# Kernel optimization log

Hardware: AMD Instinct MI355X
Metric: run time of the kernel (lower is better)

Reference implementation:

```python
import jax, jax.numpy as jnp
import numpy as np
from jax import lax

NUM_HEADS = 4
KEY_DEPTHS = 32
ATTN_CH = 32
OUT_CH = 64
IN_CH = 32
KSIZE = 3


def circ_conv3d(x, w, b=None):
    # x: (B,C,D,H,W), w: (O,I,k,k,k); circular padding keeps spatial dims.
    k = w.shape[-1]
    p = k // 2
    if p > 0:
        x = jnp.pad(x, ((0, 0), (0, 0), (p, p), (p, p), (p, p)), mode='wrap')
    y = lax.conv_general_dilated(x, w, (1, 1, 1), 'VALID',
                                 dimension_numbers=('NCDHW', 'OIDHW', 'NCDHW'))
    if b is not None:
        y = y + b[None, :, None, None, None]
    return y


def setup_inputs() -> dict:
    key = jax.random.key(0)
    k1, k2, k3, k4, k5 = jax.random.split(key, 5)
    x = jax.random.normal(k1, (2, IN_CH, 16, 16, 16), dtype=jnp.float32)
    fan = IN_CH * KSIZE ** 3
    w_init = jax.random.normal(k2, (OUT_CH - ATTN_CH, IN_CH, KSIZE, KSIZE, KSIZE), dtype=jnp.float32) / np.sqrt(fan)
    w_qkv = jax.random.normal(k3, (2 * KEY_DEPTHS + ATTN_CH, IN_CH, KSIZE, KSIZE, KSIZE), dtype=jnp.float32) / np.sqrt(fan)
    w_out = jax.random.normal(k4, (ATTN_CH, ATTN_CH, 1, 1, 1), dtype=jnp.float32) / np.sqrt(ATTN_CH)
    b_out = jax.random.normal(k5, (ATTN_CH,), dtype=jnp.float32) * 0.01
    return {'x': x, 'w_init': w_init, 'w_qkv': w_qkv, 'w_out': w_out, 'b_out': b_out}


def reference(x, w_init, w_qkv, w_out, b_out):
    out = circ_conv3d(x, w_init)                      # (b, out-attn, w,h,d)
    b, _, w, h, d = out.shape
    qkv = circ_conv3d(x, w_qkv)                       # (b, 2dk+dv, w,h,d)
    q, k, v = jnp.split(qkv, [KEY_DEPTHS, 2 * KEY_DEPTHS], axis=1)
    dk_h = KEY_DEPTHS // NUM_HEADS
    dv_h = ATTN_CH // NUM_HEADS
    N = w * h * d
    scale = dk_h ** -0.5
    fq = q.reshape(b, NUM_HEADS, dk_h, N) * scale     # (b,H,dk_h,N)
    fk = k.reshape(b, NUM_HEADS, dk_h, N)
    fv = v.reshape(b, NUM_HEADS, dv_h, N)
    logits = jnp.einsum('bhcn,bhcm->bhnm', fq, fk)    # (b,H,N,N)
    weights = jax.nn.softmax(logits, axis=-1)
    attn = jnp.einsum('bhnm,bhvm->bhnv', weights, fv)  # (b,H,N,dv_h)
    # Faithful to torch: a pure reshape (memory reinterpretation), not a transpose.
    attn = attn.reshape(b, NUM_HEADS, dv_h, w, h, d)
    attn = attn.reshape(b, NUM_HEADS * dv_h, w, h, d)  # combine heads
    attn = circ_conv3d(attn, w_out, b_out)             # 1x1x1 conv
    return jnp.concatenate([out, attn], axis=1)
```

## Files before the change

### kernel.cpp

```cpp
#include <hip/hip_runtime.h>


typedef short short8 __attribute__((ext_vector_type(8)));
typedef float float4v __attribute__((ext_vector_type(4)));
typedef unsigned short ushort_t;
typedef unsigned int uint_t;

__device__ inline ushort_t f2bf(float x) {
  uint_t u = __builtin_bit_cast(uint_t, x);
  u += 0x7FFFu + ((u >> 16) & 1u);
  return (ushort_t)(u >> 16);
}

__device__ inline uint_t cvtpk(float lo, float hi) {
  uint_t r;
  asm("v_cvt_pk_bf16_f32 %0, %1, %2" : "=v"(r) : "v"(lo), "v"(hi));
  return r;
}

__global__ __launch_bounds__(256) void kPrep(const float* __restrict__ w_init,
                                             const float* __restrict__ w_qkv,
                                             const float* __restrict__ x,
                                             ushort_t* __restrict__ wA,
                                             ushort_t* __restrict__ xb) {
  __shared__ float xsf[256 * 34];
  int t = threadIdx.x;
  int bx = blockIdx.x;
  if (bx < 432) {
    int idx = bx * 256 + t;
    int j = idx & 7;
    int lane = (idx >> 3) & 63;
    int tap = (idx >> 9) % 27;
    int otile = idx / (27 * 512);
    int o = otile * 16 + (lane & 15);
    int ic = (lane >> 4) * 8 + j;
    const float QS = 0.35355339059327373f * 1.4426950408889634f;
    float v;
    if (o < 32) v = w_init[(o * 32 + ic) * 27 + tap];
    else        v = w_qkv[((o - 32) * 32 + ic) * 27 + tap];
    if (o >= 32 && o < 64) v *= QS;
    wA[idx] = f2bf(v);
  } else {
    int bxx = bx - 432;
    int z = bxx & 15, b = bxx >> 4;
#pragma unroll
    for (int ic = 0; ic < 32; ++ic)
      xsf[t * 34 + ic] = x[((size_t)(b * 32 + ic) * 16 + z) * 256 + t];
    __syncthreads();
#pragma unroll
    for (int r = 0; r < 4; ++r) {
      int slot = r * 256 + t;
      int s = slot >> 2;
      int icg = slot & 3;
      ushort_t tmp[8];
#pragma unroll
      for (int jj = 0; jj < 8; ++jj) tmp[jj] = f2bf(xsf[s * 34 + icg * 8 + jj]);
      *(short8*)(xb + ((size_t)(b * 16 + z) * 256 + s) * 32 + icg * 8) = *(short8*)tmp;
    }
  }
}

__global__ __launch_bounds__(256, 1) void kConv(const ushort_t* __restrict__ xb,
                                                const ushort_t* __restrict__ wA,
                                                float* __restrict__ out,
                                                ushort_t* __restrict__ Qbf,
                                                ushort_t* __restrict__ Kbf,
                                                ushort_t* __restrict__ VtTp) {
  __shared__ ushort_t xs[3 * 256 * 32];
  int tid = threadIdx.x;
  int w = tid >> 6, lane = tid & 63;
  int quad = lane >> 4, nl = lane & 15;
  int bx = blockIdx.x;
  int oq = bx & 3;
  int z = (bx >> 2) & 15;
  int b = bx >> 6;

#pragma unroll
  for (int j = 0; j < 12; ++j) {
    int idx = j * 256 + tid;
    int p = idx >> 10;
    int rem = idx & 1023;
    int zr = (z + p + 15) & 15;
    *(short8*)(xs + p * 8192 + rem * 8) =
        *(const short8*)(xb + (size_t)(b * 16 + zr) * 8192 + rem * 8);
  }
  __syncthreads();

  float4v acc[2][4];
#pragma unroll
  for (int ot = 0; ot < 2; ++ot)
#pragma unroll
    for (int st = 0; st < 4; ++st) acc[ot][st] = (float4v){0.f, 0.f, 0.f, 0.f};

  int y0 = w * 4;
  for (int tap = 0; tap < 27; ++tap) {
    int kz = tap / 9, kyx = tap % 9;
    int ky = kyx / 3, kx = kyx % 3;
    short8 afrag[2];
#pragma unroll
    for (int ot = 0; ot < 2; ++ot)
      afrag[ot] = *(const short8*)(wA + ((size_t)((oq * 2 + ot) * 27 + tap) * 64 + lane) * 8);
    int xsh = (nl + kx + 15) & 15;
#pragma unroll
    for (int st = 0; st < 4; ++st) {
      int yy = (y0 + st + ky + 15) & 15;
      short8 bfrag = *(const short8*)(xs + ((kz * 256) + yy * 16 + xsh) * 32 + quad * 8);
#pragma unroll
      for (int ot = 0; ot < 2; ++ot)
        acc[ot][st] = __builtin_amdgcn_mfma_f32_16x16x32_bf16(afrag[ot], bfrag, acc[ot][st], 0, 0, 0);
    }
  }

#pragma unroll
  for (int st = 0; st < 4; ++st) {
    int y = y0 + st;
    int s = z * 256 + y * 16 + nl;
    int mperm = 2 * nl + (y & 1);
#pragma unroll
    for (int ot = 0; ot < 2; ++ot) {
      int otg = oq * 2 + ot;
#pragma unroll
      for (int r = 0; r < 4; ++r) {
        float val = acc[ot][st][r];
        int oo = (otg & 1) * 16 + quad * 4 + r;
        if (otg < 2) {
          out[(size_t)(b * 64 + oo) * 4096 + s] = val;
        } else if (otg < 4) {
          int h = oo >> 3, c = oo & 7;
          Qbf[((size_t)(b * 4 + h) * 4096 + s) * 8 + c] = f2bf(val);
        } else if (otg < 6) {
          int h = oo >> 3, c = oo & 7;
          Kbf[((size_t)(b * 4 + h) * 4096 + s) * 8 + c] = f2bf(val);
        } else {
          int h = oo >> 3, c = oo & 7;
          VtTp[((size_t)(b * 4 + h) * 8 + c) * 4096 + (size_t)(s & ~31) + mperm] = f2bf(val);
        }
      }
    }
  }
}

__global__ __launch_bounds__(256) void kAttn(const ushort_t* __restrict__ Qbf,
                                             const ushort_t* __restrict__ Kbf,
                                             const ushort_t* __restrict__ VtTp,
                                             float* __restrict__ pacc,
                                             float* __restrict__ pl) {
  __shared__ ushort_t Plds[4 * 2 * 2 * 640];
  int tid = threadIdx.x;
  int w = tid >> 6, lane = tid & 63;
  int id = blockIdx.x * 4 + w;
  int bh = id >> 9;
  int ksp = (id >> 7) & 3;
  int ntile = id & 127;
  int n0 = ntile * 32;
  int quad = lane >> 4, nl = lane & 15;
  int l31 = lane & 31;
  int v = nl;

  short8 z8 = {};
  short8 q0f = *(const short8*)(Qbf + ((size_t)bh * 4096 + n0 + nl) * 8);
  short8 q1f = *(const short8*)(Qbf + ((size_t)bh * 4096 + n0 + 16 + nl) * 8);
  short8 aq0A = (quad == 0) ? q0f : z8;
  short8 aq0B = (quad == 1) ? q0f : z8;
  short8 aq1A = (quad == 0) ? q1f : z8;
  short8 aq1B = (quad == 1) ? q1f : z8;

  short8 ones8;
#pragma unroll
  for (int i = 0; i < 8; ++i) ones8[i] = (short)0x3F80;

  const ushort_t* Krows = Kbf + ((size_t)bh * 4096 + ksp * 1024) * 8;
  const ushort_t* Vrow = VtTp + ((size_t)bh * 8 + (v < 8 ? v : 0)) * 4096
                         + ksp * 1024 + quad * 8;
  ushort_t* P0 = Plds + (w * 2 + 0) * 2 * 640;
  ushort_t* P1 = Plds + (w * 2 + 1) * 2 * 640;

  float4v acc0 = {}, acc1 = {};

#define QKEXP(mi, bkr)                                                         \
  {                                                                            \
    float4v s00 = __builtin_amdgcn_mfma_f32_16x16x32_bf16(                     \
        aq0A, bkr, (float4v){0.f, 0.f, 0.f, 0.f}, 0, 0, 0);                    \
    float4v s01 = __builtin_amdgcn_mfma_f32_16x16x32_bf16(                     \
        aq0B, bkr, (float4v){0.f, 0.f, 0.f, 0.f}, 0, 0, 0);                    \
    float4v s10 = __builtin_amdgcn_mfma_f32_16x16x32_bf16(                     \
        aq1A, bkr, (float4v){0.f, 0.f, 0.f, 0.f}, 0, 0, 0);                    \
    float4v s11 = __builtin_amdgcn_mfma_f32_16x16x32_bf16(                     \
        aq1B, bkr, (float4v){0.f, 0.f, 0.f, 0.f}, 0, 0, 0);                    \
    uint_t* Pt0 = (uint_t*)(P0 + ((mi) & 1) * 640);                            \
    uint_t* Pt1 = (uint_t*)(P1 + ((mi) & 1) * 640);                            \
    _Pragma("unroll") for (int r = 0; r < 4; ++r) {                            \
      Pt0[(quad * 4 + r) * 20 + nl] =                                          \
          cvtpk(__builtin_amdgcn_exp2f(s00[r]), __builtin_amdgcn_exp2f(s01[r]));\
      Pt1[(quad * 4 + r) * 20 + nl] =                                          \
          cvtpk(__builtin_amdgcn_exp2f(s10[r]), __builtin_amdgcn_exp2f(s11[r]));\
    }                                                                          \
  }

#define PVSTEP(a2, bv, accv)                                                   \
  {                                                                            \
    short8 b2 = (v < 8) ? (bv) : ((v == 8) ? ones8 : z8);                      \
    accv = __builtin_amdgcn_mfma_f32_16x16x32_bf16(a2, b2, accv, 0, 0, 0);     \
  }

  short8 bk = *(const short8*)(Krows + (size_t)l31 * 8);
  QKEXP(0, bk)
  bk = *(const short8*)(Krows + (size_t)(32 + l31) * 8);

#pragma unroll 2
  for (int mi = 1; mi < 32; ++mi) {
    int pb = ((mi - 1) & 1) * 640;
    short8 a20 = *(const short8*)(P0 + pb + nl * 40 + quad * 8);
    short8 a21 = *(const short8*)(P1 + pb + nl * 40 + quad * 8);
    short8 bv = *(const short8*)(Vrow + (mi - 1) * 32);
    QKEXP(mi, bk)
    int nxt = ((mi + 1) & 31) * 32;
    bk = *(const short8*)(Krows + (size_t)(nxt + l31) * 8);
    PVSTEP(a20, bv, acc0)
    PVSTEP(a21, bv, acc1)
  }
  {
    int pb = 640;
    short8 a20 = *(const short8*)(P0 + pb + nl * 40 + quad * 8);
    short8 a21 = *(const short8*)(P1 + pb + nl * 40 + quad * 8);
    short8 bv = *(const short8*)(Vrow + 31 * 32);
    PVSTEP(a20, bv, acc0)
    PVSTEP(a21, bv, acc1)
  }
#undef QKEXP
#undef PVSTEP

#pragma unroll
  for (int r = 0; r < 4; ++r) {
    int rq = quad * 4 + r;
    int rowg0 = bh * 4096 + n0 + rq;
    int rowg1 = rowg0 + 16;
    if (v < 8) {
      pacc[((size_t)rowg0 * 4 + ksp) * 8 + v] = acc0[r];
      pacc[((size_t)rowg1 * 4 + ksp) * 8 + v] = acc1[r];
    } else if (v == 8) {
      pl[(size_t)rowg0 * 4 + ksp] = acc0[r];
      pl[(size_t)rowg1 * 4 + ksp] = acc1[r];
    }
  }
}

__global__ __launch_bounds__(256) void kMerge(const float* __restrict__ pacc,
                                              const float* __restrict__ pl,
                                              float* __restrict__ attn) {
  int idx = blockIdx.x * 256 + threadIdx.x;
  int row = idx >> 3;
  int c = idx & 7;
  float l = 0.f, a = 0.f;
#pragma unroll
  for (int s = 0; s < 4; ++s) {
    l += pl[(size_t)row * 4 + s];
    a += pacc[((size_t)row * 4 + s) * 8 + c];
  }
  int b = row >> 14;
  int h = (row >> 12) & 3;
  int n = row & 4095;
  attn[((size_t)(b * 32 + h * 8 + (n >> 9)) << 12) + ((n & 511) * 8 + c)] = a / l;
}

__global__ __launch_bounds__(256) void kOut(const float* __restrict__ attn,
                                            const float* __restrict__ w_out,
                                            const float* __restrict__ b_out,
                                            float* __restrict__ out) {
  int idx = blockIdx.x * 256 + threadIdx.x;
  int s = idx & 4095;
  int b = (idx >> 12) & 1;
  int cp = idx >> 13;
  float a[32];
#pragma unroll
  for (int ci = 0; ci < 32; ++ci) a[ci] = attn[(size_t)(b * 32 + ci) * 4096 + s];
#pragma unroll
  for (int oo = 0; oo < 2; ++oo) {
    int co = cp * 2 + oo;
    float r = b_out[co];
#pragma unroll
    for (int ci = 0; ci < 32; ++ci) r = fmaf(w_out[co * 32 + ci], a[ci], r);
    out[(size_t)(b * 64 + 32 + co) * 4096 + s] = r;
  }
}

extern "C" void kernel_launch(void* const* d_in, const int* in_sizes, int n_in,
                              void* d_out, int out_size, void* d_ws, size_t ws_size,
                              hipStream_t stream) {
  const float* x      = (const float*)d_in[0];
  const float* w_init = (const float*)d_in[1];
  const float* w_qkv  = (const float*)d_in[2];
  const float* w_out  = (const float*)d_in[3];
  const float* b_out  = (const float*)d_in[4];
  float* out = (float*)d_out;

  ushort_t* wA  = (ushort_t*)d_ws;
  ushort_t* xb  = wA + 110592;
  ushort_t* Qbf = xb + 262144;
  ushort_t* Kbf = Qbf + 262144;
  ushort_t* VtTp = Kbf + 262144;
  float* attn = (float*)(VtTp + 262144);
  float* pacc = attn + 262144;
  float* pl = pacc + 1048576;

  kPrep <<<464,  256, 0, stream>>>(w_init, w_qkv, x, wA, xb);
  kConv <<<128,  256, 0, stream>>>(xb, wA, out, Qbf, Kbf, VtTp);
  kAttn <<<1024, 256, 0, stream>>>(Qbf, Kbf, VtTp, pacc, pl);
  kMerge<<<1024, 256, 0, stream>>>(pacc, pl, attn);
  kOut  <<<512,  256, 0, stream>>>(attn, w_out, b_out, out);
}
```

Measured before the change: 109.7 us.

## Split attention keys eight ways and fuse merge into output projection

The attention kernel now splits the key dimension into 8 chunks instead of 4, doubling the grid to 2048 blocks with half the loop length each. This gives more parallelism across the GPU's compute units. The separate merge kernel is removed: the 1x1 output conv kernel now sums the partial accumulators and denominators, normalizes, stages the 32-channel tile in LDS, and applies the projection. This drops one launch and the intermediate attn buffer round trip. The cost is doubled partial-result traffic and a fused kernel with only 128 blocks.

```diff
diff --git a/kernel.cpp b/kernel.cpp
--- a/kernel.cpp
+++ b/kernel.cpp
@@ -149,8 +149,8 @@
   int tid = threadIdx.x;
   int w = tid >> 6, lane = tid & 63;
   int id = blockIdx.x * 4 + w;
-  int bh = id >> 9;
-  int ksp = (id >> 7) & 3;
+  int bh = id >> 10;
+  int ksp = (id >> 7) & 7;
   int ntile = id & 127;
   int n0 = ntile * 32;
   int quad = lane >> 4, nl = lane & 15;
@@ -169,9 +169,9 @@
 #pragma unroll
   for (int i = 0; i < 8; ++i) ones8[i] = (short)0x3F80;
 
-  const ushort_t* Krows = Kbf + ((size_t)bh * 4096 + ksp * 1024) * 8;
+  const ushort_t* Krows = Kbf + ((size_t)bh * 4096 + ksp * 512) * 8;
   const ushort_t* Vrow = VtTp + ((size_t)bh * 8 + (v < 8 ? v : 0)) * 4096
-                         + ksp * 1024 + quad * 8;
+                         + ksp * 512 + quad * 8;
   ushort_t* P0 = Plds + (w * 2 + 0) * 2 * 640;
   ushort_t* P1 = Plds + (w * 2 + 1) * 2 * 640;
 
@@ -208,13 +208,13 @@
   bk = *(const short8*)(Krows + (size_t)(32 + l31) * 8);
 
 #pragma unroll 2
-  for (int mi = 1; mi < 32; ++mi) {
+  for (int mi = 1; mi < 16; ++mi) {
     int pb = ((mi - 1) & 1) * 640;
     short8 a20 = *(const short8*)(P0 + pb + nl * 40 + quad * 8);
     short8 a21 = *(const short8*)(P1 + pb + nl * 40 + quad * 8);
     short8 bv = *(const short8*)(Vrow + (mi - 1) * 32);
     QKEXP(mi, bk)
-    int nxt = ((mi + 1) & 31) * 32;
+    int nxt = ((mi + 1) & 15) * 32;
     bk = *(const short8*)(Krows + (size_t)(nxt + l31) * 8);
     PVSTEP(a20, bv, acc0)
     PVSTEP(a21, bv, acc1)
@@ -223,7 +223,7 @@
     int pb = 640;
     short8 a20 = *(const short8*)(P0 + pb + nl * 40 + quad * 8);
     short8 a21 = *(const short8*)(P1 + pb + nl * 40 + quad * 8);
-    short8 bv = *(const short8*)(Vrow + 31 * 32);
+    short8 bv = *(const short8*)(Vrow + 15 * 32);
     PVSTEP(a20, bv, acc0)
     PVSTEP(a21, bv, acc1)
   }
@@ -236,51 +236,66 @@
     int rowg0 = bh * 4096 + n0 + rq;
     int rowg1 = rowg0 + 16;
     if (v < 8) {
-      pacc[((size_t)rowg0 * 4 + ksp) * 8 + v] = acc0[r];
-      pacc[((size_t)rowg1 * 4 + ksp) * 8 + v] = acc1[r];
+      pacc[((size_t)rowg0 * 8 + ksp) * 8 + v] = acc0[r];
+      pacc[((size_t)rowg1 * 8 + ksp) * 8 + v] = acc1[r];
     } else if (v == 8) {
-      pl[(size_t)rowg0 * 4 + ksp] = acc0[r];
-      pl[(size_t)rowg1 * 4 + ksp] = acc1[r];
-    }
-  }
-}
-
-__global__ __launch_bounds__(256) void kMerge(const float* __restrict__ pacc,
-                                              const float* __restrict__ pl,
-                                              float* __restrict__ attn) {
-  int idx = blockIdx.x * 256 + threadIdx.x;
-  int row = idx >> 3;
-  int c = idx & 7;
-  float l = 0.f, a = 0.f;
-#pragma unroll
-  for (int s = 0; s < 4; ++s) {
-    l += pl[(size_t)row * 4 + s];
-    a += pacc[((size_t)row * 4 + s) * 8 + c];
-  }
-  int b = row >> 14;
-  int h = (row >> 12) & 3;
-  int n = row & 4095;
-  attn[((size_t)(b * 32 + h * 8 + (n >> 9)) << 12) + ((n & 511) * 8 + c)] = a / l;
-}
-
-__global__ __launch_bounds__(256) void kOut(const float* __restrict__ attn,
+      pl[(size_t)rowg0 * 8 + ksp] = acc0[r];
+      pl[(size_t)rowg1 * 8 + ksp] = acc1[r];
+    }
+  }
+}
+
+__global__ __launch_bounds__(256) void kOut(const float* __restrict__ pacc,
+                                            const float* __restrict__ pl,
                                             const float* __restrict__ w_out,
                                             const float* __restrict__ b_out,
                                             float* __restrict__ out) {
-  int idx = blockIdx.x * 256 + threadIdx.x;
-  int s = idx & 4095;
-  int b = (idx >> 12) & 1;
-  int cp = idx >> 13;
-  float a[32];
-#pragma unroll
-  for (int ci = 0; ci < 32; ++ci) a[ci] = attn[(size_t)(b * 32 + ci) * 4096 + s];
-#pragma unroll
-  for (int oo = 0; oo < 2; ++oo) {
-    int co = cp * 2 + oo;
-    float r = b_out[co];
-#pragma unroll
-    for (int ci = 0; ci < 32; ++ci) r = fmaf(w_out[co * 32 + ci], a[ci], r);
-    out[(size_t)(b * 64 + 32 + co) * 4096 + s] = r;
+  __shared__ float M[32 * 64];
+  int bx = blockIdx.x;
+  int b = bx >> 6;
+  int sp0 = (bx & 63) * 64;
+  int t = threadIdx.x;
+
+  {
+    int ci = t >> 3, nsub = t & 7;
+    int h = ci >> 3, tt = ci & 7;
+    int n = tt * 512 + (sp0 >> 3) + nsub;
+    size_t row = (size_t)(b * 4 + h) * 4096 + n;
+    float l = 0.f;
+#pragma unroll
+    for (int s = 0; s < 8; ++s) l += pl[row * 8 + s];
+    float rl = 1.0f / l;
+    float m[8];
+#pragma unroll
+    for (int c = 0; c < 8; ++c) m[c] = 0.f;
+#pragma unroll
+    for (int s = 0; s < 8; ++s) {
+      const float4 p0 = *(const float4*)(pacc + (row * 8 + s) * 8);
+      const float4 p1 = *(const float4*)(pacc + (row * 8 + s) * 8 + 4);
+      m[0] += p0.x; m[1] += p0.y; m[2] += p0.z; m[3] += p0.w;
+      m[4] += p1.x; m[5] += p1.y; m[6] += p1.z; m[7] += p1.w;
+    }
+    float4 o0 = {m[0] * rl, m[1] * rl, m[2] * rl, m[3] * rl};
+    float4 o1 = {m[4] * rl, m[5] * rl, m[6] * rl, m[7] * rl};
+    *(float4*)(M + ci * 64 + nsub * 8) = o0;
+    *(float4*)(M + ci * 64 + nsub * 8 + 4) = o1;
+  }
+  __syncthreads();
+
+  {
+    int spl = t & 63;
+    int cog = t >> 6;
+    float a[32];
+#pragma unroll
+    for (int ci = 0; ci < 32; ++ci) a[ci] = M[ci * 64 + spl];
+#pragma unroll
+    for (int oo = 0; oo < 8; ++oo) {
+      int co = cog * 8 + oo;
+      float r = b_out[co];
+#pragma unroll
+      for (int ci = 0; ci < 32; ++ci) r = fmaf(w_out[co * 32 + ci], a[ci], r);
+      out[(size_t)(b * 64 + 32 + co) * 4096 + sp0 + spl] = r;
+    }
   }
 }
 
@@ -299,13 +314,11 @@
   ushort_t* Qbf = xb + 262144;
   ushort_t* Kbf = Qbf + 262144;
   ushort_t* VtTp = Kbf + 262144;
-  float* attn = (float*)(VtTp + 262144);
-  float* pacc = attn + 262144;
-  float* pl = pacc + 1048576;
+  float* pacc = (float*)(VtTp + 262144);
+  float* pl = pacc + 2097152;
 
   kPrep <<<464,  256, 0, stream>>>(w_init, w_qkv, x, wA, xb);
   kConv <<<128,  256, 0, stream>>>(xb, wA, out, Qbf, Kbf, VtTp);
-  kAttn <<<1024, 256, 0, stream>>>(Qbf, Kbf, VtTp, pacc, pl);
-  kMerge<<<1024, 256, 0, stream>>>(pacc, pl, attn);
-  kOut  <<<512,  256, 0, stream>>>(attn, w_out, b_out, out);
-}
+  kAttn <<<2048, 256, 0, stream>>>(Qbf, Kbf, VtTp, pacc, pl);
+  kOut  <<<128,  256, 0, stream>>>(pacc, pl, w_out, b_out, out);
+}
```

After: 109.5 us. No clear change (-0.1%).
